# Performance work log

Measured on AMD Instinct MI355X. Metric: run time of the kernel, lower is better.

## Reference

```python
import jax, jax.numpy as jnp
import numpy as np

N, M, D, DV = 8192, 8192, 64, 64

def setup_inputs() -> dict:
    key = jax.random.key(0)
    kq, kk, kv = jax.random.split(key, 3)
    Q = jax.random.normal(kq, (N, D), dtype=jnp.float32)
    K = jax.random.normal(kk, (M, D), dtype=jnp.float32)
    V = jax.random.normal(kv, (M, DV), dtype=jnp.float32)
    return {"Q": Q, "K": K, "V": V}

def reference(Q, K, V):
    d = K.shape[-1]
    scores = jnp.einsum('nd,md->nm', Q, K) / jnp.sqrt(jnp.float32(d))  # [N, M]
    attn = jax.nn.softmax(scores, axis=-1)
    return attn @ V  # [N, DV]
```

## Files before the change

kernel.cpp:

```cpp
#include <hip/hip_runtime.h>


#define NQ 8192
#define NK 8192

typedef float f32x4 __attribute__((ext_vector_type(4)));
typedef short short8 __attribute__((ext_vector_type(8)));
union U4 { uint4 u; short8 s; };

#define MFMA16 __builtin_amdgcn_mfma_f32_16x16x32_bf16

__device__ __forceinline__ unsigned pk2(float a, float b) {
    unsigned ua = __builtin_bit_cast(unsigned, a);
    unsigned ub = __builtin_bit_cast(unsigned, b);
    ua = (ua + 0x7FFFu + ((ua >> 16) & 1u)) >> 16;
    ub = (ub + 0x7FFFu + ((ub >> 16) & 1u)) & 0xFFFF0000u;
    return ua | ub;
}

__device__ __forceinline__ unsigned pkt(float a, float b) {
    return __builtin_amdgcn_perm(__builtin_bit_cast(unsigned, b),
                                 __builtin_bit_cast(unsigned, a), 0x07060302u);
}

__global__ __launch_bounds__(256)
void prepass(const float* __restrict__ Kg, const float* __restrict__ Vg,
             uint4* __restrict__ Kb4, uint4* __restrict__ Vt4) {
    __shared__ float ld[64 * 33];
    const int t = threadIdx.x, b = blockIdx.x;

    if (b < 256) {
        const int kl = t >> 3, dg = t & 7;
        const int e = kl & 1, i16 = kl >> 1, h = dg >> 2, q = dg & 3;
        const float* gp = Kg + (size_t)(b * 32 + kl) * 64 + dg * 8;
        float4 f0 = *(const float4*)gp;
        float4 f1 = *(const float4*)(gp + 4);
        uint4 o = make_uint4(pk2(f0.x, f0.y), pk2(f0.z, f0.w),
                             pk2(f1.x, f1.y), pk2(f1.z, f1.w));
        Kb4[(size_t)(b * 4 + e * 2 + h) * 64 + i16 * 4 + q] = o;
    } else {
        const int c = b - 256;
        {
            const int key = t >> 3, dg = t & 7;
            const float* gp = Vg + (size_t)(c * 32 + key) * 64 + dg * 8;
            float4 f0 = *(const float4*)gp;
            float4 f1 = *(const float4*)(gp + 4);
            ld[(dg * 8 + 0) * 33 + key] = f0.x;
            ld[(dg * 8 + 1) * 33 + key] = f0.y;
            ld[(dg * 8 + 2) * 33 + key] = f0.z;
            ld[(dg * 8 + 3) * 33 + key] = f0.w;
            ld[(dg * 8 + 4) * 33 + key] = f1.x;
            ld[(dg * 8 + 5) * 33 + key] = f1.y;
            ld[(dg * 8 + 6) * 33 + key] = f1.z;
            ld[(dg * 8 + 7) * 33 + key] = f1.w;
        }
        __syncthreads();
        {
            const int dim = t >> 2, kq = t & 3;
            const int dt = dim >> 4, i16 = dim & 15;
            float v[8];
            #pragma unroll
            for (int j = 0; j < 8; ++j) v[j] = ld[dim * 33 + kq * 8 + j];
            uint4 o = make_uint4(pk2(v[0], v[1]), pk2(v[2], v[3]),
                                 pk2(v[4], v[5]), pk2(v[6], v[7]));
            Vt4[(size_t)(c * 4 + dt) * 64 + i16 * 4 + kq] = o;
        }
    }
}

__global__ __launch_bounds__(512, 1)
void attn_main(const float* __restrict__ Qg,
               const uint4* __restrict__ Kb4,
               const uint4* __restrict__ Vt4,
               float* __restrict__ Opart,
               float* __restrict__ Lpart) {
    __shared__ uint4 shb4[4160];
    float* sF = (float*)shb4;
    unsigned* shu = (unsigned*)shb4;

    const int t = threadIdx.x, w = t >> 6, lane = t & 63;
    const int q = lane >> 4, i16 = lane & 15;
    const int bid = blockIdx.x;
    const int kh = bid & 1;
    const int rg = bid >> 1;
    const int qb0 = rg * 64;
    const int lsl = i16 * 4 + q;
    const int phase = rg & 15;

    const float SCL = 0.18033688011112042f;
    short8 aq[4][2];
    #pragma unroll
    for (int rt = 0; rt < 4; ++rt) {
        const float* qp = Qg + (size_t)(qb0 + rt * 16 + i16) * 64 + q * 8;
        float4 f0 = *(const float4*)(qp);
        float4 f1 = *(const float4*)(qp + 4);
        U4 u;
        u.u = make_uint4(pk2(f0.x * SCL, f0.y * SCL), pk2(f0.z * SCL, f0.w * SCL),
                         pk2(f1.x * SCL, f1.y * SCL), pk2(f1.z * SCL, f1.w * SCL));
        aq[rt][0] = u.s;
        f0 = *(const float4*)(qp + 32);
        f1 = *(const float4*)(qp + 36);
        u.u = make_uint4(pk2(f0.x * SCL, f0.y * SCL), pk2(f0.z * SCL, f0.w * SCL),
                         pk2(f1.x * SCL, f1.y * SCL), pk2(f1.z * SCL, f1.w * SCL));
        aq[rt][1] = u.s;
    }

    f32x4 acc[4][4];
    float lsum[4][4];
    #pragma unroll
    for (int rt = 0; rt < 4; ++rt) {
        #pragma unroll
        for (int dt = 0; dt < 4; ++dt) { acc[rt][dt][0]=0.f; acc[rt][dt][1]=0.f; acc[rt][dt][2]=0.f; acc[rt][dt][3]=0.f; }
        #pragma unroll
        for (int r = 0; r < 4; ++r) lsum[rt][r] = 0.f;
    }

    const int tpw = ((i16 >> 2) & 1) + 2 * q + 32 * (i16 >> 3);
    const int pp  = i16 & 3;
    const int tpr = (q & 1) + 2 * ((i16 >> 2) & 3) + 8 * (i16 & 3) + 32 * (q >> 1);

    uint4 kfA[4], vfA[4], kfB[4], vfB[4];

#define LOAD_T(TT, KD, VD)                                                           \
    do {                                                                             \
        const int cb = ((kh << 7) + ((((TT) + phase) & 15) * 8 + w)) * 4;            \
        _Pragma("unroll")                                                            \
        for (int eh = 0; eh < 4; ++eh)                                               \
            (KD)[eh] = Kb4[(size_t)(cb + eh) * 64 + lsl];                            \
        _Pragma("unroll")                                                            \
        for (int dt = 0; dt < 4; ++dt)                                               \
            (VD)[dt] = Vt4[(size_t)(cb + dt) * 64 + lsl];                            \
    } while (0)

#define QKEXP(KD, PAR)                                                               \
    do {                                                                             \
        _Pragma("unroll")                                                            \
        for (int rt = 0; rt < 4; ++rt) {                                             \
            f32x4 s0, s1;                                                            \
            s0[0]=-16.f; s0[1]=-16.f; s0[2]=-16.f; s0[3]=-16.f;                      \
            s1[0]=-16.f; s1[1]=-16.f; s1[2]=-16.f; s1[3]=-16.f;                      \
            U4 u0, u1, u2, u3;                                                       \
            u0.u = (KD)[0]; u1.u = (KD)[1]; u2.u = (KD)[2]; u3.u = (KD)[3];          \
            s0 = MFMA16(aq[rt][0], u0.s, s0, 0, 0, 0);                               \
            s0 = MFMA16(aq[rt][1], u1.s, s0, 0, 0, 0);                               \
            s1 = MFMA16(aq[rt][0], u2.s, s1, 0, 0, 0);                               \
            s1 = MFMA16(aq[rt][1], u3.s, s1, 0, 0, 0);                               \
            const int rbase = (((w * 4 + rt) * 2) + (PAR)) * 256;                    \
            _Pragma("unroll")                                                        \
            for (int r = 0; r < 4; ++r) {                                            \
                float p0 = __builtin_amdgcn_exp2f(s0[r]);                            \
                float p1 = __builtin_amdgcn_exp2f(s1[r]);                            \
                lsum[rt][r] += p0;                                                   \
                lsum[rt][r] += p1;                                                   \
                shu[rbase + (tpw + 8 * r) * 4 + pp] = pkt(p0, p1);                   \
            }                                                                        \
        }                                                                            \
    } while (0)

#define PVS(VD, PAR)                                                                 \
    do {                                                                             \
        U4 ap[4];                                                                    \
        _Pragma("unroll")                                                            \
        for (int rt = 0; rt < 4; ++rt)                                               \
            ap[rt].u = shb4[(((w * 4 + rt) * 2) + (PAR)) * 64 + tpr];                \
        _Pragma("unroll")                                                            \
        for (int dt = 0; dt < 4; ++dt) {                                             \
            U4 bv; bv.u = (VD)[dt];                                                  \
            _Pragma("unroll")                                                        \
            for (int rt = 0; rt < 4; ++rt)                                           \
                acc[rt][dt] = MFMA16(ap[rt].s, bv.s, acc[rt][dt], 0, 0, 0);          \
        }                                                                            \
    } while (0)

    LOAD_T(0, kfA, vfA);
    LOAD_T(1, kfB, vfB);
    QKEXP(kfA, 0);
    #pragma unroll 1
    for (int tt = 1; tt < 15; tt += 2) {
        QKEXP(kfB, 1);
        PVS(vfA, 0);
        LOAD_T(tt + 1, kfA, vfA);
        QKEXP(kfA, 0);
        PVS(vfB, 1);
        LOAD_T(tt + 2, kfB, vfB);
        __builtin_amdgcn_sched_barrier(0);
    }
    QKEXP(kfB, 1);
    PVS(vfA, 0);
    PVS(vfB, 1);

    #pragma unroll
    for (int rt = 0; rt < 4; ++rt)
        #pragma unroll
        for (int r = 0; r < 4; ++r) {
            float v = lsum[rt][r];
            v += __shfl_xor(v, 1);
            v += __shfl_xor(v, 2);
            v += __shfl_xor(v, 4);
            v += __shfl_xor(v, 8);
            lsum[rt][r] = v;
        }

    __syncthreads();
    for (int step = 4; step >= 1; step >>= 1) {
        if (w >= step && w < 2 * step) {
            float* base = sF + (w - step) * 4160;
            #pragma unroll
            for (int rt = 0; rt < 4; ++rt) {
                #pragma unroll
                for (int dt = 0; dt < 4; ++dt)
                    #pragma unroll
                    for (int r = 0; r < 4; ++r)
                        base[(rt * 16 + 4 * q + r) * 64 + dt * 16 + i16] = acc[rt][dt][r];
                if (i16 == 0) {
                    #pragma unroll
                    for (int r = 0; r < 4; ++r) base[4096 + rt * 16 + 4 * q + r] = lsum[rt][r];
                }
            }
        }
        __syncthreads();
        if (w < step) {
            const float* base = sF + w * 4160;
            #pragma unroll
            for (int rt = 0; rt < 4; ++rt) {
                #pragma unroll
                for (int dt = 0; dt < 4; ++dt)
                    #pragma unroll
                    for (int r = 0; r < 4; ++r)
                        acc[rt][dt][r] += base[(rt * 16 + 4 * q + r) * 64 + dt * 16 + i16];
                #pragma unroll
                for (int r = 0; r < 4; ++r) lsum[rt][r] += base[4096 + rt * 16 + 4 * q + r];
            }
        }
        __syncthreads();
    }

    if (w == 0) {
        #pragma unroll
        for (int rt = 0; rt < 4; ++rt) {
            #pragma unroll
            for (int dt = 0; dt < 4; ++dt)
                #pragma unroll
                for (int r = 0; r < 4; ++r) {
                    const int row = qb0 + rt * 16 + 4 * q + r;
                    Opart[((size_t)kh * 8192 + row) * 64 + dt * 16 + i16] = acc[rt][dt][r];
                }
            if (i16 == 0) {
                #pragma unroll
                for (int r = 0; r < 4; ++r)
                    Lpart[kh * 8192 + qb0 + rt * 16 + 4 * q + r] = lsum[rt][r];
            }
        }
    }
}

__global__ __launch_bounds__(256)
void merge(const float* __restrict__ Opart, const float* __restrict__ Lpart,
           float* __restrict__ Og) {
    const int idx = blockIdx.x * 256 + threadIdx.x;
    const int row = idx >> 4, seg = idx & 15;
    const float4 a = *(const float4*)(Opart + (size_t)row * 64 + seg * 4);
    const float4 b = *(const float4*)(Opart + ((size_t)8192 + row) * 64 + seg * 4);
    const float inv = 1.0f / (Lpart[row] + Lpart[8192 + row]);
    float4 o;
    o.x = (a.x + b.x) * inv;
    o.y = (a.y + b.y) * inv;
    o.z = (a.z + b.z) * inv;
    o.w = (a.w + b.w) * inv;
    *(float4*)(Og + (size_t)row * 64 + seg * 4) = o;
}

extern "C" void kernel_launch(void* const* d_in, const int* in_sizes, int n_in,
                              void* d_out, int out_size, void* d_ws, size_t ws_size,
                              hipStream_t stream) {
    const float* Q = (const float*)d_in[0];
    const float* K = (const float*)d_in[1];
    const float* V = (const float*)d_in[2];
    float* O = (float*)d_out;
    char* ws = (char*)d_ws;
    uint4* Kb4   = (uint4*)ws;
    uint4* Vt4   = (uint4*)(ws + (1 << 20));
    float* Opart = (float*)(ws + (2 << 20));
    float* Lpart = (float*)(ws + (6 << 20));
    hipLaunchKernelGGL(prepass, dim3(512), dim3(256), 0, stream, K, V, Kb4, Vt4);
    hipLaunchKernelGGL(attn_main, dim3(256), dim3(512), 0, stream, Q, Kb4, Vt4, Opart, Lpart);
    hipLaunchKernelGGL(merge, dim3(512), dim3(256), 0, stream, Opart, Lpart, O);
}
```

Measured before the change: 89.20 us.

## Halve query rows per block, double grid, and shrink V register double-buffering

Each block now handles 32 query rows instead of 64, so the grid grows from 256 to 512 blocks and each wave keeps half the accumulator and Q-fragment registers. Launch bounds are raised to allow 4 blocks per CU and shared memory is halved to match. V fragments are no longer double-buffered; a single vf buffer is reloaded just before use while K stays double-buffered, with an adjusted prologue and epilogue. The aim is higher occupancy and better use of all CUs, at the cost of reloading each K/V tile for twice as many blocks, less register prefetch of V, and more reduction and merge overhead per output row.

After: 104.1 us. 1.17x slower.

```diff
diff --git a/kernel.cpp b/kernel.cpp
--- a/kernel.cpp
+++ b/kernel.cpp
@@ -68,13 +68,13 @@
     }
 }
 
-__global__ __launch_bounds__(512, 1)
+__global__ __launch_bounds__(512, 4)
 void attn_main(const float* __restrict__ Qg,
                const uint4* __restrict__ Kb4,
                const uint4* __restrict__ Vt4,
                float* __restrict__ Opart,
                float* __restrict__ Lpart) {
-    __shared__ uint4 shb4[4160];
+    __shared__ uint4 shb4[2080];
     float* sF = (float*)shb4;
     unsigned* shu = (unsigned*)shb4;
 
@@ -83,14 +83,42 @@
     const int bid = blockIdx.x;
     const int kh = bid & 1;
     const int rg = bid >> 1;
-    const int qb0 = rg * 64;
+    const int qb0 = rg * 32;
     const int lsl = i16 * 4 + q;
     const int phase = rg & 15;
 
+    const int tpw = ((i16 >> 2) & 1) + 2 * q + 32 * (i16 >> 3);
+    const int pp  = i16 & 3;
+    const int tpr = (q & 1) + 2 * ((i16 >> 2) & 3) + 8 * (i16 & 3) + 32 * (q >> 1);
+
+    uint4 kfA[4], kfB[4], vf[4];
+
+#define CBASE(TT) (((kh << 7) + ((((TT) + phase) & 15) * 8 + w)) * 4)
+
+#define LOAD_K(KD, TT)                                                               \
+    do {                                                                             \
+        const int cb = CBASE(TT);                                                    \
+        _Pragma("unroll")                                                            \
+        for (int eh = 0; eh < 4; ++eh)                                               \
+            (KD)[eh] = Kb4[(size_t)(cb + eh) * 64 + lsl];                            \
+    } while (0)
+
+#define LOAD_V(TT)                                                                   \
+    do {                                                                             \
+        const int cb = CBASE(TT);                                                    \
+        _Pragma("unroll")                                                            \
+        for (int dt = 0; dt < 4; ++dt)                                               \
+            vf[dt] = Vt4[(size_t)(cb + dt) * 64 + lsl];                              \
+    } while (0)
+
+    LOAD_K(kfA, 0);
+    LOAD_V(0);
+    LOAD_K(kfB, 1);
+
     const float SCL = 0.18033688011112042f;
-    short8 aq[4][2];
+    short8 aq[2][2];
     #pragma unroll
-    for (int rt = 0; rt < 4; ++rt) {
+    for (int rt = 0; rt < 2; ++rt) {
         const float* qp = Qg + (size_t)(qb0 + rt * 16 + i16) * 64 + q * 8;
         float4 f0 = *(const float4*)(qp);
         float4 f1 = *(const float4*)(qp + 4);
@@ -105,37 +133,20 @@
         aq[rt][1] = u.s;
     }
 
-    f32x4 acc[4][4];
-    float lsum[4][4];
+    f32x4 acc[2][4];
+    float lsum[2][4];
     #pragma unroll
-    for (int rt = 0; rt < 4; ++rt) {
+    for (int rt = 0; rt < 2; ++rt) {
         #pragma unroll
         for (int dt = 0; dt < 4; ++dt) { acc[rt][dt][0]=0.f; acc[rt][dt][1]=0.f; acc[rt][dt][2]=0.f; acc[rt][dt][3]=0.f; }
         #pragma unroll
         for (int r = 0; r < 4; ++r) lsum[rt][r] = 0.f;
     }
 
-    const int tpw = ((i16 >> 2) & 1) + 2 * q + 32 * (i16 >> 3);
-    const int pp  = i16 & 3;
-    const int tpr = (q & 1) + 2 * ((i16 >> 2) & 3) + 8 * (i16 & 3) + 32 * (q >> 1);
-
-    uint4 kfA[4], vfA[4], kfB[4], vfB[4];
-
-#define LOAD_T(TT, KD, VD)                                                           \
-    do {                                                                             \
-        const int cb = ((kh << 7) + ((((TT) + phase) & 15) * 8 + w)) * 4;            \
-        _Pragma("unroll")                                                            \
-        for (int eh = 0; eh < 4; ++eh)                                               \
-            (KD)[eh] = Kb4[(size_t)(cb + eh) * 64 + lsl];                            \
-        _Pragma("unroll")                                                            \
-        for (int dt = 0; dt < 4; ++dt)                                               \
-            (VD)[dt] = Vt4[(size_t)(cb + dt) * 64 + lsl];                            \
-    } while (0)
-
 #define QKEXP(KD, PAR)                                                               \
     do {                                                                             \
         _Pragma("unroll")                                                            \
-        for (int rt = 0; rt < 4; ++rt) {                                             \
+        for (int rt = 0; rt < 2; ++rt) {                                             \
             f32x4 s0, s1;                                                            \
             s0[0]=-16.f; s0[1]=-16.f; s0[2]=-16.f; s0[3]=-16.f;                      \
             s1[0]=-16.f; s1[1]=-16.f; s1[2]=-16.f; s1[3]=-16.f;                      \
@@ -145,7 +156,7 @@
             s0 = MFMA16(aq[rt][1], u1.s, s0, 0, 0, 0);                               \
             s1 = MFMA16(aq[rt][0], u2.s, s1, 0, 0, 0);                               \
             s1 = MFMA16(aq[rt][1], u3.s, s1, 0, 0, 0);                               \
-            const int rbase = (((w * 4 + rt) * 2) + (PAR)) * 256;                    \
+            const int rbase = (((w * 2 + rt) * 2) + (PAR)) * 256;                    \
             _Pragma("unroll")                                                        \
             for (int r = 0; r < 4; ++r) {                                            \
                 float p0 = __builtin_amdgcn_exp2f(s0[r]);                            \
@@ -157,40 +168,49 @@
         }                                                                            \
     } while (0)
 
-#define PVS(VD, PAR)                                                                 \
+#define PVS(PAR)                                                                     \
     do {                                                                             \
-        U4 ap[4];                                                                    \
-        _Pragma("unroll")                                                            \
-        for (int rt = 0; rt < 4; ++rt)                                               \
-            ap[rt].u = shb4[(((w * 4 + rt) * 2) + (PAR)) * 64 + tpr];                \
+        U4 ap[2];                                                                    \
+        _Pragma("unroll")                                                            \
+        for (int rt = 0; rt < 2; ++rt)                                               \
+            ap[rt].u = shb4[(((w * 2 + rt) * 2) + (PAR)) * 64 + tpr];                \
         _Pragma("unroll")                                                            \
         for (int dt = 0; dt < 4; ++dt) {                                             \
-            U4 bv; bv.u = (VD)[dt];                                                  \
+            U4 bv; bv.u = vf[dt];                                                    \
             _Pragma("unroll")                                                        \
-            for (int rt = 0; rt < 4; ++rt)                                           \
+            for (int rt = 0; rt < 2; ++rt)                                           \
                 acc[rt][dt] = MFMA16(ap[rt].s, bv.s, acc[rt][dt], 0, 0, 0);          \
         }                                                                            \
     } while (0)
 
-    LOAD_T(0, kfA, vfA);
-    LOAD_T(1, kfB, vfB);
     QKEXP(kfA, 0);
+    LOAD_K(kfA, 2);
     #pragma unroll 1
-    for (int tt = 1; tt < 15; tt += 2) {
+    for (int tt = 1; tt < 13; tt += 2) {
         QKEXP(kfB, 1);
-        PVS(vfA, 0);
-        LOAD_T(tt + 1, kfA, vfA);
+        PVS(0);
+        LOAD_K(kfB, tt + 2);
+        LOAD_V(tt);
         QKEXP(kfA, 0);
-        PVS(vfB, 1);
-        LOAD_T(tt + 2, kfB, vfB);
+        PVS(1);
+        LOAD_K(kfA, tt + 3);
+        LOAD_V(tt + 1);
         __builtin_amdgcn_sched_barrier(0);
     }
     QKEXP(kfB, 1);
-    PVS(vfA, 0);
-    PVS(vfB, 1);
+    PVS(0);
+    LOAD_K(kfB, 15);
+    LOAD_V(13);
+    QKEXP(kfA, 0);
+    PVS(1);
+    LOAD_V(14);
+    QKEXP(kfB, 1);
+    PVS(0);
+    LOAD_V(15);
+    PVS(1);
 
     #pragma unroll
-    for (int rt = 0; rt < 4; ++rt)
+    for (int rt = 0; rt < 2; ++rt)
         #pragma unroll
         for (int r = 0; r < 4; ++r) {
             float v = lsum[rt][r];
@@ -204,9 +224,9 @@
     __syncthreads();
     for (int step = 4; step >= 1; step >>= 1) {
         if (w >= step && w < 2 * step) {
-            float* base = sF + (w - step) * 4160;
+            float* base = sF + (w - step) * 2080;
             #pragma unroll
-            for (int rt = 0; rt < 4; ++rt) {
+            for (int rt = 0; rt < 2; ++rt) {
                 #pragma unroll
                 for (int dt = 0; dt < 4; ++dt)
                     #pragma unroll
@@ -214,22 +234,22 @@
                         base[(rt * 16 + 4 * q + r) * 64 + dt * 16 + i16] = acc[rt][dt][r];
                 if (i16 == 0) {
                     #pragma unroll
-                    for (int r = 0; r < 4; ++r) base[4096 + rt * 16 + 4 * q + r] = lsum[rt][r];
+                    for (int r = 0; r < 4; ++r) base[2048 + rt * 16 + 4 * q + r] = lsum[rt][r];
                 }
             }
         }
         __syncthreads();
         if (w < step) {
-            const float* base = sF + w * 4160;
+            const float* base = sF + w * 2080;
             #pragma unroll
-            for (int rt = 0; rt < 4; ++rt) {
+            for (int rt = 0; rt < 2; ++rt) {
                 #pragma unroll
                 for (int dt = 0; dt < 4; ++dt)
                     #pragma unroll
                     for (int r = 0; r < 4; ++r)
                         acc[rt][dt][r] += base[(rt * 16 + 4 * q + r) * 64 + dt * 16 + i16];
                 #pragma unroll
-                for (int r = 0; r < 4; ++r) lsum[rt][r] += base[4096 + rt * 16 + 4 * q + r];
+                for (int r = 0; r < 4; ++r) lsum[rt][r] += base[2048 + rt * 16 + 4 * q + r];
             }
         }
         __syncthreads();
@@ -237,7 +257,7 @@
 
     if (w == 0) {
         #pragma unroll
-        for (int rt = 0; rt < 4; ++rt) {
+        for (int rt = 0; rt < 2; ++rt) {
             #pragma unroll
             for (int dt = 0; dt < 4; ++dt)
                 #pragma unroll
@@ -283,6 +303,6 @@
     float* Opart = (float*)(ws + (2 << 20));
     float* Lpart = (float*)(ws + (6 << 20));
     hipLaunchKernelGGL(prepass, dim3(512), dim3(256), 0, stream, K, V, Kb4, Vt4);
-    hipLaunchKernelGGL(attn_main, dim3(256), dim3(512), 0, stream, Q, Kb4, Vt4, Opart, Lpart);
+    hipLaunchKernelGGL(attn_main, dim3(512), dim3(512), 0, stream, Q, Kb4, Vt4, Opart, Lpart);
     hipLaunchKernelGGL(merge, dim3(512), dim3(256), 0, stream, Opart, Lpart, O);
 }
```
